# Optimization experiments

Hardware: AMD Instinct MI355X
Metric: run time of the kernel (lower is better)

## Reference

```python
import jax, jax.numpy as jnp
import numpy as np

IN_DIM, HID, OUT, B, MAX_LEN = 164, 512, 1, 1024, 128


def _uni(key, shape, fan_in):
    b = 1.0 / np.sqrt(fan_in)
    return jax.random.uniform(key, shape, jnp.float32, -b, b)


def setup_inputs() -> dict:
    rng = np.random.default_rng(0)
    sizes = rng.integers(1, MAX_LEN, size=B)  # lengths in [1, 127]
    T = int(sizes.sum())  # total ragged tokens (~65k)
    key = jax.random.key(0)
    ks = jax.random.split(key, 16)
    return {
        "segment_sizes": jnp.asarray(sizes, jnp.int32),
        "features": jax.random.normal(ks[0], (T, IN_DIM), jnp.float32),
        # encoder MLP: Linear(in,hid) -> ReLU -> Linear(hid,hid) -> ReLU
        "We0": _uni(ks[1], (HID, IN_DIM), IN_DIM), "be0": _uni(ks[2], (HID,), IN_DIM),
        "We1": _uni(ks[3], (HID, HID), HID),       "be1": _uni(ks[4], (HID,), HID),
        # single-layer LSTM, torch gate order (i, f, g, o)
        "Wih": _uni(ks[5], (4 * HID, HID), HID),   "bih": _uni(ks[6], (4 * HID,), HID),
        "Whh": _uni(ks[7], (4 * HID, HID), HID),   "bhh": _uni(ks[8], (4 * HID,), HID),
        # residual MLPs l0, l1
        "Wl0": _uni(ks[9], (HID, HID), HID),  "bl0": _uni(ks[10], (HID,), HID),
        "Wl1": _uni(ks[11], (HID, HID), HID), "bl1": _uni(ks[12], (HID,), HID),
        # decoder Linear(hid, out)
        "Wd": _uni(ks[13], (OUT, HID), HID), "bd": _uni(ks[14], (OUT,), HID),
    }


def reference(segment_sizes, features, We0, be0, We1, be1,
              Wih, bih, Whh, bhh, Wl0, bl0, Wl1, bl1, Wd, bd):
    T = features.shape[0]
    # segment encoder MLP on ragged tokens
    x = jax.nn.relu(features @ We0.T + be0)
    x = jax.nn.relu(x @ We1.T + be1)  # [T, HID]
    # pad_sequence: scatter ragged tokens into [MAX_LEN, B, HID] (zero padded)
    starts = jnp.cumsum(segment_sizes) - segment_sizes
    seg = jnp.repeat(jnp.arange(B), segment_sizes, total_repeat_length=T)
    pos = jnp.arange(T) - starts[seg]
    padded = jnp.zeros((MAX_LEN, B, HID), x.dtype).at[pos, seg].set(x)

    # LSTM scan; note: original runs the LSTM over padded zeros too and takes
    # h after the full MAX_LEN steps (no packing) -- reproduce that exactly.
    def step(carry, xt):
        h, c = carry
        g = xt @ Wih.T + bih + h @ Whh.T + bhh  # [B, 4H]
        i, f, gg, o = jnp.split(g, 4, axis=-1)
        c = jax.nn.sigmoid(f) * c + jax.nn.sigmoid(i) * jnp.tanh(gg)
        h = jax.nn.sigmoid(o) * jnp.tanh(c)
        return (h, c), None

    zeros = jnp.zeros((B, HID), x.dtype)
    (h, _), _ = jax.lax.scan(step, (zeros, zeros), padded)

    out = h  # norm is Identity
    out = jax.nn.relu(out @ Wl0.T + bl0) + out
    out = jax.nn.relu(out @ Wl1.T + bl1) + out
    out = (out @ Wd.T + bd).squeeze()  # [B]
    return out
```

## Files before the change

### kernel.cpp

```cpp
#include <hip/hip_runtime.h>
#include <hip/hip_bf16.h>

typedef __attribute__((ext_vector_type(8))) short short8;
typedef __attribute__((ext_vector_type(4))) float f32x4;

#define DEV __device__ __forceinline__

DEV short f2bf(float f){ __hip_bfloat16 h = __float2bfloat16(f); return *reinterpret_cast<short*>(&h); }
DEV float bf2f(short s){ __hip_bfloat16 h; *reinterpret_cast<short*>(&h) = s; return __bfloat162float(h); }

DEV float sigm(float x){ return 1.f/(1.f + __expf(-x)); }
DEV float tanh_f(float x){
  float ax = fabsf(x);
  float e = __expf(-2.f*ax);
  float t = (1.f - e)/(1.f + e);
  return copysignf(t, x);
}

DEV short8 llc_ld16(const short* p){
  union { unsigned long long u[2]; short8 v; } r;
  r.u[0] = __hip_atomic_load((const unsigned long long*)p,
                             __ATOMIC_RELAXED, __HIP_MEMORY_SCOPE_AGENT);
  r.u[1] = __hip_atomic_load((const unsigned long long*)(p + 4),
                             __ATOMIC_RELAXED, __HIP_MEMORY_SCOPE_AGENT);
  return r.v;
}


__global__ void k_cvt(const float* __restrict__ in, short* __restrict__ out, long n){
  long i = (long)blockIdx.x*blockDim.x + threadIdx.x;
  long st = (long)gridDim.x*blockDim.x;
  for (; i < n; i += st) out[i] = f2bf(in[i]);
}

__global__ void k_cvt_pad(const float* __restrict__ in, short* __restrict__ out,
                          int rows, int ic, int oc){
  long n = (long)rows*oc;
  long st = (long)gridDim.x*blockDim.x;
  for (long i = (long)blockIdx.x*blockDim.x + threadIdx.x; i < n; i += st){
    int r = (int)(i / oc), c = (int)(i % oc);
    out[i] = (c < ic) ? f2bf(in[(long)r*ic + c]) : (short)0;
  }
}

__global__ void k_bias2(const float* __restrict__ a, const float* __restrict__ b,
                        float* __restrict__ o, int n){
  int i = blockIdx.x*blockDim.x + threadIdx.x;
  if (i < n) o[i] = a[i] + b[i];
}

__global__ void k_scan(const int* __restrict__ sizes, int* __restrict__ starts, int B){
  __shared__ int t[1024];
  int tid = threadIdx.x;
  int v = (tid < B) ? sizes[tid] : 0;
  t[tid] = v;
  __syncthreads();
  for (int off = 1; off < 1024; off <<= 1){
    int add = (tid >= off) ? t[tid-off] : 0;
    __syncthreads();
    t[tid] += add;
    __syncthreads();
  }
  if (tid < B) starts[tid] = t[tid] - v;
}

template<bool RELU, bool RESID, bool OBF, bool OF32, bool AF32>
__global__ __launch_bounds__(256) void k_gemm(
    const void* __restrict__ Araw, int lda, int Ktrue,
    const short* __restrict__ Bw, int ldb,
    const float* __restrict__ bias,
    const float* __restrict__ R,
    short* __restrict__ Cb, float* __restrict__ Cf, int ldc,
    int M, int N, int K)
{
  constexpr int BM = 64, BN = 128, BK = 64;
  __shared__ short lA[(BK/8)*BM*8];
  __shared__ short lB[(BK/8)*BN*8];
  const short* Ab = (const short*)Araw;
  const float* Af = (const float*)Araw;
  const int tid = threadIdx.x;
  const int l = tid & 63, w = tid >> 6;
  const int lr = l & 15, lk = l >> 4;
  const int bm0 = blockIdx.x*BM, bn0 = blockIdx.y*BN;

  f32x4 acc[4][2];
  #pragma unroll
  for (int a = 0; a < 4; a++)
    #pragma unroll
    for (int b = 0; b < 2; b++) acc[a][b] = (f32x4){0.f,0.f,0.f,0.f};

  for (int k0 = 0; k0 < K; k0 += BK){
    #pragma unroll
    for (int i = 0; i < 2; i++){
      int idx = tid + i*256;
      int m = idx >> 3, kc = idx & 7;
      int gm = bm0 + m; if (gm >= M) gm = M-1;
      short8 v;
      if (AF32){
        int kb = k0 + kc*8;
        if (kb + 8 <= Ktrue){
          const float* p = Af + (long)gm*lda + kb;
          float4 f0 = *(const float4*)p;
          float4 f1 = *(const float4*)(p + 4);
          v[0]=f2bf(f0.x); v[1]=f2bf(f0.y); v[2]=f2bf(f0.z); v[3]=f2bf(f0.w);
          v[4]=f2bf(f1.x); v[5]=f2bf(f1.y); v[6]=f2bf(f1.z); v[7]=f2bf(f1.w);
        } else {
          #pragma unroll
          for (int e = 0; e < 8; e++){
            int k = kb + e;
            v[e] = (k < Ktrue) ? f2bf(Af[(long)gm*lda + k]) : (short)0;
          }
        }
      } else {
        v = *(const short8*)(Ab + (long)gm*lda + k0 + kc*8);
      }
      *(short8*)&lA[(kc*BM + m)*8] = v;
    }
    #pragma unroll
    for (int i = 0; i < 4; i++){
      int idx = tid + i*256;
      int n = idx >> 3, kc = idx & 7;
      *(short8*)&lB[(kc*BN + n)*8] = *(const short8*)(Bw + (long)(bn0+n)*ldb + k0 + kc*8);
    }
    __syncthreads();
    #pragma unroll
    for (int kb = 0; kb < 2; kb++){
      short8 af[4], bfv[2];
      #pragma unroll
      for (int mf = 0; mf < 4; mf++)
        af[mf] = *(short8*)&lA[((kb*4+lk)*BM + mf*16 + lr)*8];
      #pragma unroll
      for (int nf = 0; nf < 2; nf++)
        bfv[nf] = *(short8*)&lB[((kb*4+lk)*BN + w*32 + nf*16 + lr)*8];
      #pragma unroll
      for (int mf = 0; mf < 4; mf++)
        #pragma unroll
        for (int nf = 0; nf < 2; nf++)
          acc[mf][nf] = __builtin_amdgcn_mfma_f32_16x16x32_bf16(af[mf], bfv[nf], acc[mf][nf], 0, 0, 0);
    }
    __syncthreads();
  }

  #pragma unroll
  for (int mf = 0; mf < 4; mf++){
    #pragma unroll
    for (int nf = 0; nf < 2; nf++){
      #pragma unroll
      for (int r = 0; r < 4; r++){
        int row = bm0 + mf*16 + lk*4 + r;
        int col = bn0 + w*32 + nf*16 + lr;
        if (row < M){
          float v = acc[mf][nf][r];
          if (bias) v += bias[col];
          if (RELU) v = fmaxf(v, 0.f);
          if (RESID) v += R[(long)row*ldc + col];
          if (OBF) Cb[(long)row*ldc + col] = f2bf(v);
          if (OF32) Cf[(long)row*ldc + col] = v;
        }
      }
    }
  }
}

__global__ __launch_bounds__(256, 1) void k_lstm(
    const short* __restrict__ Whh,
    const short* __restrict__ Wih,
    const short* __restrict__ Xt,
    short* __restrict__ h0, short* __restrict__ h1,
    float* __restrict__ hF,
    const int* __restrict__ sizes, const int* __restrict__ starts,
    const float* __restrict__ bias2, unsigned int* __restrict__ cnt)
{
  __shared__ short wx[4*2*16*64*8];
  const int bid = blockIdx.x;
  const int xcd = bid & 7;
  const int q   = bid >> 3;
  const int ht  = q & 15;
  const int bm  = ((q >> 4) << 3) | xcd;
  const int tid = threadIdx.x;
  const int l = tid & 63, wid = tid >> 6;
  const int wr = wid >> 1, wc = wid & 1;
  const int lr = l & 15, lk = l >> 4;
  const int rowbase = bm*64 + wr*32;
  const int j = ht*32 + wc*16 + lr;

  for (int c = tid; c < 8192; c += 256){
    int lane = c & 63;
    int kk  = (c >> 6) & 15;
    int wcs = (c >> 10) & 1;
    int g   = c >> 11;
    int row = g*512 + ht*32 + wcs*16 + (lane & 15);
    int col = kk*32 + (lane >> 4)*8;
    *(short8*)&wx[(size_t)c*8] = *(const short8*)(Wih + (long)row*512 + col);
  }

  short8 Breg[4][16];
  #pragma unroll
  for (int g = 0; g < 4; ++g){
    const short* wp = Whh + (long)(g*512 + j)*512 + lk*8;
    #pragma unroll
    for (int kk = 0; kk < 16; ++kk)
      Breg[g][kk] = *(const short8*)(wp + kk*32);
  }

  float bz[4];
  #pragma unroll
  for (int g = 0; g < 4; ++g) bz[g] = bias2[g*512 + j];

  const int len0 = sizes[rowbase + lr];
  const int len1 = sizes[rowbase + 16 + lr];
  const long xb0 = (long)starts[rowbase + lr]*512;
  const long xb1 = (long)starts[rowbase + 16 + lr]*512;

  __syncthreads();

  float cst[2][4] = {{0.f,0.f,0.f,0.f},{0.f,0.f,0.f,0.f}};
  const int cidx = bm*128;
  const short8 z8 = {0,0,0,0,0,0,0,0};
  const int wxw = wc*16*64*8;

  #pragma unroll 1
  for (int t = 0; t < 128; ++t){
    const short* hc = (t & 1) ? h1 : h0;
    short*       hn = (t & 1) ? h0 : h1;
    const bool on0 = t < len0, on1 = t < len1;
    const short* px0 = Xt + xb0 + (on0 ? (long)t*512 : 0) + lk*8;
    const short* px1 = Xt + xb1 + (on1 ? (long)t*512 : 0) + lk*8;

    f32x4 acc[2][4];
    #pragma unroll
    for (int mf = 0; mf < 2; ++mf)
      #pragma unroll
      for (int g = 0; g < 4; ++g) acc[mf][g] = (f32x4){0.f,0.f,0.f,0.f};

    #pragma unroll
    for (int kk = 0; kk < 16; ++kk){
      short8 x0 = on0 ? *(const short8*)(px0 + kk*32) : z8;
      short8 x1 = on1 ? *(const short8*)(px1 + kk*32) : z8;
      #pragma unroll
      for (int g = 0; g < 4; ++g){
        short8 bx = *(short8*)&wx[g*(2*16*64*8) + wxw + (kk*64 + l)*8];
        acc[0][g] = __builtin_amdgcn_mfma_f32_16x16x32_bf16(x0, bx, acc[0][g], 0, 0, 0);
        acc[1][g] = __builtin_amdgcn_mfma_f32_16x16x32_bf16(x1, bx, acc[1][g], 0, 0, 0);
      }
    }

    if (t > 0){
      if (tid == 0){
        while (__hip_atomic_load(&cnt[cidx + t - 1], __ATOMIC_RELAXED,
                                 __HIP_MEMORY_SCOPE_AGENT) < 16u)
          __builtin_amdgcn_s_sleep(1);
      }
      __syncthreads();
      asm volatile("" ::: "memory");
      __builtin_amdgcn_sched_barrier(0);

      const short* ph = hc + (long)(rowbase + lr)*512 + lk*8;
      #pragma unroll
      for (int kk = 0; kk < 16; ++kk){
        short8 a0 = llc_ld16(ph + kk*32);
        short8 a1 = llc_ld16(ph + 16*512 + kk*32);
        #pragma unroll
        for (int g = 0; g < 4; ++g){
          acc[0][g] = __builtin_amdgcn_mfma_f32_16x16x32_bf16(a0, Breg[g][kk], acc[0][g], 0, 0, 0);
          acc[1][g] = __builtin_amdgcn_mfma_f32_16x16x32_bf16(a1, Breg[g][kk], acc[1][g], 0, 0, 0);
        }
      }
    }

    #pragma unroll
    for (int mf = 0; mf < 2; ++mf)
      #pragma unroll
      for (int r = 0; r < 4; ++r){
        int rb = rowbase + mf*16 + lk*4 + r;
        float ip = acc[mf][0][r] + bz[0];
        float fp = acc[mf][1][r] + bz[1];
        float gp = acc[mf][2][r] + bz[2];
        float op = acc[mf][3][r] + bz[3];
        float cn = sigm(fp)*cst[mf][r] + sigm(ip)*tanh_f(gp);
        float hv = sigm(op)*tanh_f(cn);
        cst[mf][r] = cn;
        unsigned int x16 = (unsigned short)f2bf(hv);
        unsigned int par = (unsigned int)__shfl_xor((int)x16, 1, 64);
        if (!(lr & 1)){
          unsigned int wv = x16 | (par << 16);
          __hip_atomic_store((unsigned int*)(hn + (long)rb*512 + (j & ~1)), wv,
                             __ATOMIC_RELAXED, __HIP_MEMORY_SCOPE_AGENT);
        }
        if (t == 127) hF[(long)rb*512 + j] = hv;
      }

    asm volatile("s_waitcnt vmcnt(0) lgkmcnt(0)" ::: "memory");
    __syncthreads();
    if (tid == 0)
      __hip_atomic_fetch_add(&cnt[cidx + t], 1u, __ATOMIC_RELAXED,
                             __HIP_MEMORY_SCOPE_AGENT);
  }
}

__global__ __launch_bounds__(256) void k_dec(const float* __restrict__ X,
                                             const float* __restrict__ Wd,
                                             const float* __restrict__ bd,
                                             float* __restrict__ out, int B){
  int w = threadIdx.x >> 6, l = threadIdx.x & 63;
  int row = blockIdx.x*4 + w;
  if (row >= B) return;
  float s = 0.f;
  #pragma unroll
  for (int e = 0; e < 8; e++){
    int j = l + 64*e;
    s += X[(long)row*512 + j]*Wd[j];
  }
  #pragma unroll
  for (int off = 32; off > 0; off >>= 1) s += __shfl_down(s, off);
  if (l == 0) out[row] = s + bd[0];
}


extern "C" void kernel_launch(void* const* d_in, const int* in_sizes, int n_in,
                              void* d_out, int out_size, void* d_ws, size_t ws_size,
                              hipStream_t stream)
{
  const int*   sizes = (const int*)  d_in[0];
  const float* feat  = (const float*)d_in[1];
  const float* We0   = (const float*)d_in[2];
  const float* be0   = (const float*)d_in[3];
  const float* We1   = (const float*)d_in[4];
  const float* be1   = (const float*)d_in[5];
  const float* Wih   = (const float*)d_in[6];
  const float* bih   = (const float*)d_in[7];
  const float* Whh   = (const float*)d_in[8];
  const float* bhh   = (const float*)d_in[9];
  const float* Wl0   = (const float*)d_in[10];
  const float* bl0   = (const float*)d_in[11];
  const float* Wl1   = (const float*)d_in[12];
  const float* bl1   = (const float*)d_in[13];
  const float* Wd    = (const float*)d_in[14];
  const float* bd    = (const float*)d_in[15];

  const int B = in_sizes[0];
  const int T = in_sizes[1] / 164;
  const int HID = 512;

  char* base = (char*)d_ws;
  size_t off = 0;
  auto alloc = [&](size_t bytes)->char*{
    char* p = base + off;
    off = (off + bytes + 255) & ~(size_t)255;
    return p;
  };

  int*          starts = (int*)         alloc((size_t)B*4);
  float*        bias2  = (float*)       alloc(2048*4);
  unsigned int* cnt    = (unsigned int*)alloc(16*128*4);
  short* We0b   = (short*)alloc((size_t)512*192*2);
  short* We1b   = (short*)alloc((size_t)512*512*2);
  short* Wihb   = (short*)alloc((size_t)2048*512*2);
  short* Whhb   = (short*)alloc((size_t)2048*512*2);
  short* Wl0b   = (short*)alloc((size_t)512*512*2);
  short* Wl1b   = (short*)alloc((size_t)512*512*2);
  short* hA     = (short*)alloc((size_t)B*HID*2);
  short* hB     = (short*)alloc((size_t)B*HID*2);
  float* hF     = (float*)alloc((size_t)B*HID*4);
  float* r1     = (float*)alloc((size_t)B*HID*4);
  short* r1b    = (short*)alloc((size_t)B*HID*2);
  float* r2     = (float*)alloc((size_t)B*HID*4);
  short* X0b    = (short*)alloc((size_t)T*512*2);
  short* Xb     = (short*)alloc((size_t)T*512*2);
  (void)ws_size; (void)n_in; (void)out_size;

  hipMemsetAsync(cnt, 0, (size_t)16*128*4, stream);

  k_scan<<<1, 1024, 0, stream>>>(sizes, starts, B);
  k_bias2<<<8, 256, 0, stream>>>(bih, bhh, bias2, 2048);

  auto grd = [](long n){ long g = (n + 255)/256; return (int)(g > 4096 ? 4096 : g); };
  k_cvt_pad<<<grd(512l*192), 256, 0, stream>>>(We0, We0b, 512, 164, 192);
  k_cvt<<<grd(512l*512), 256, 0, stream>>>(We1, We1b, 512l*512);
  k_cvt<<<grd(2048l*512), 256, 0, stream>>>(Wih, Wihb, 2048l*512);
  k_cvt<<<grd(2048l*512), 256, 0, stream>>>(Whh, Whhb, 2048l*512);
  k_cvt<<<grd(512l*512), 256, 0, stream>>>(Wl0, Wl0b, 512l*512);
  k_cvt<<<grd(512l*512), 256, 0, stream>>>(Wl1, Wl1b, 512l*512);

  int mt = (T + 63)/64;
  k_gemm<true,false,true,false,true><<<dim3(mt, 4), 256, 0, stream>>>(
      (const void*)feat, 164, 164, We0b, 192, be0, nullptr, X0b, nullptr, 512, T, 512, 192);
  k_gemm<true,false,true,false,false><<<dim3(mt, 4), 256, 0, stream>>>(
      (const void*)X0b, 512, 512, We1b, 512, be1, nullptr, Xb, nullptr, 512, T, 512, 512);

  k_lstm<<<256, 256, 0, stream>>>(Whhb, Wihb, Xb, hA, hB, hF,
                                  sizes, starts, bias2, cnt);

  k_gemm<true,true,true,true,true><<<dim3(16, 4), 256, 0, stream>>>(
      (const void*)hF, 512, 512, Wl0b, 512, bl0, hF, r1b, r1, 512, B, 512, 512);
  k_gemm<true,true,false,true,false><<<dim3(16, 4), 256, 0, stream>>>(
      (const void*)r1b, 512, 512, Wl1b, 512, bl1, r1, nullptr, r2, 512, B, 512, 512);

  k_dec<<<B/4, 256, 0, stream>>>(r2, Wd, bd, (float*)d_out, B);
}
```

Measured before the change: 2.293 ms.

## Replace per-step atomic counter with per-block step flags and batch h loads

The cross-block LSTM step barrier changes from a shared atomic counter incremented by each of 16 blocks to per-block flag words that each block overwrites with its step number. A whole wavefront polls the 16 flags in parallel, which avoids contention from atomic read-modify-write. The h loads are also hoisted ahead of the MFMA loop so all global loads issue before any compute, and the final step skips the h store and barrier. Holding all h loads in flight raises register pressure in a kernel already keeping Whh in registers.

```diff
diff --git a/kernel.cpp b/kernel.cpp
--- a/kernel.cpp
+++ b/kernel.cpp
@@ -169,7 +169,7 @@
     short* __restrict__ h0, short* __restrict__ h1,
     float* __restrict__ hF,
     const int* __restrict__ sizes, const int* __restrict__ starts,
-    const float* __restrict__ bias2, unsigned int* __restrict__ cnt)
+    const float* __restrict__ bias2, unsigned int* __restrict__ flags)
 {
   __shared__ short wx[4*2*16*64*8];
   const int bid = blockIdx.x;
@@ -183,6 +183,7 @@
   const int lr = l & 15, lk = l >> 4;
   const int rowbase = bm*64 + wr*32;
   const int j = ht*32 + wc*16 + lr;
+  const int fb = bm*16;
 
   for (int c = tid; c < 8192; c += 256){
     int lane = c & 63;
@@ -215,7 +216,6 @@
   __syncthreads();
 
   float cst[2][4] = {{0.f,0.f,0.f,0.f},{0.f,0.f,0.f,0.f}};
-  const int cidx = bm*128;
   const short8 z8 = {0,0,0,0,0,0,0,0};
   const int wxw = wc*16*64*8;
 
@@ -246,24 +246,32 @@
     }
 
     if (t > 0){
-      if (tid == 0){
-        while (__hip_atomic_load(&cnt[cidx + t - 1], __ATOMIC_RELAXED,
-                                 __HIP_MEMORY_SCOPE_AGENT) < 16u)
-          __builtin_amdgcn_s_sleep(1);
+      if (wid == 0){
+        const unsigned int want = (unsigned int)t;
+        while (true){
+          unsigned int v = __hip_atomic_load(&flags[fb + (l & 15)],
+                                             __ATOMIC_RELAXED, __HIP_MEMORY_SCOPE_AGENT);
+          if (__all(v >= want)) break;
+          __builtin_amdgcn_s_sleep(2);
+        }
       }
       __syncthreads();
       asm volatile("" ::: "memory");
       __builtin_amdgcn_sched_barrier(0);
 
       const short* ph = hc + (long)(rowbase + lr)*512 + lk*8;
+      short8 ha0[16], ha1[16];
       #pragma unroll
       for (int kk = 0; kk < 16; ++kk){
-        short8 a0 = llc_ld16(ph + kk*32);
-        short8 a1 = llc_ld16(ph + 16*512 + kk*32);
+        ha0[kk] = llc_ld16(ph + kk*32);
+        ha1[kk] = llc_ld16(ph + 16*512 + kk*32);
+      }
+      #pragma unroll
+      for (int kk = 0; kk < 16; ++kk){
         #pragma unroll
         for (int g = 0; g < 4; ++g){
-          acc[0][g] = __builtin_amdgcn_mfma_f32_16x16x32_bf16(a0, Breg[g][kk], acc[0][g], 0, 0, 0);
-          acc[1][g] = __builtin_amdgcn_mfma_f32_16x16x32_bf16(a1, Breg[g][kk], acc[1][g], 0, 0, 0);
+          acc[0][g] = __builtin_amdgcn_mfma_f32_16x16x32_bf16(ha0[kk], Breg[g][kk], acc[0][g], 0, 0, 0);
+          acc[1][g] = __builtin_amdgcn_mfma_f32_16x16x32_bf16(ha1[kk], Breg[g][kk], acc[1][g], 0, 0, 0);
         }
       }
     }
@@ -280,21 +288,26 @@
         float cn = sigm(fp)*cst[mf][r] + sigm(ip)*tanh_f(gp);
         float hv = sigm(op)*tanh_f(cn);
         cst[mf][r] = cn;
-        unsigned int x16 = (unsigned short)f2bf(hv);
-        unsigned int par = (unsigned int)__shfl_xor((int)x16, 1, 64);
-        if (!(lr & 1)){
-          unsigned int wv = x16 | (par << 16);
-          __hip_atomic_store((unsigned int*)(hn + (long)rb*512 + (j & ~1)), wv,
-                             __ATOMIC_RELAXED, __HIP_MEMORY_SCOPE_AGENT);
+        if (t < 127){
+          unsigned int x16 = (unsigned short)f2bf(hv);
+          unsigned int par = (unsigned int)__shfl_xor((int)x16, 1, 64);
+          if (!(lr & 1)){
+            unsigned int wv = x16 | (par << 16);
+            __hip_atomic_store((unsigned int*)(hn + (long)rb*512 + (j & ~1)), wv,
+                               __ATOMIC_RELAXED, __HIP_MEMORY_SCOPE_AGENT);
+          }
+        } else {
+          hF[(long)rb*512 + j] = hv;
         }
-        if (t == 127) hF[(long)rb*512 + j] = hv;
-      }
-
-    asm volatile("s_waitcnt vmcnt(0) lgkmcnt(0)" ::: "memory");
-    __syncthreads();
-    if (tid == 0)
-      __hip_atomic_fetch_add(&cnt[cidx + t], 1u, __ATOMIC_RELAXED,
-                             __HIP_MEMORY_SCOPE_AGENT);
+      }
+
+    if (t < 127){
+      asm volatile("s_waitcnt vmcnt(0) lgkmcnt(0)" ::: "memory");
+      __syncthreads();
+      if (tid == 0)
+        __hip_atomic_store(&flags[fb + ht], (unsigned int)(t + 1),
+                           __ATOMIC_RELAXED, __HIP_MEMORY_SCOPE_AGENT);
+    }
   }
 }
 
@@ -352,7 +365,7 @@
 
   int*          starts = (int*)         alloc((size_t)B*4);
   float*        bias2  = (float*)       alloc(2048*4);
-  unsigned int* cnt    = (unsigned int*)alloc(16*128*4);
+  unsigned int* flags  = (unsigned int*)alloc(256*4);
   short* We0b   = (short*)alloc((size_t)512*192*2);
   short* We1b   = (short*)alloc((size_t)512*512*2);
   short* Wihb   = (short*)alloc((size_t)2048*512*2);
@@ -369,7 +382,7 @@
   short* Xb     = (short*)alloc((size_t)T*512*2);
   (void)ws_size; (void)n_in; (void)out_size;
 
-  hipMemsetAsync(cnt, 0, (size_t)16*128*4, stream);
+  hipMemsetAsync(flags, 0, 256*4, stream);
 
   k_scan<<<1, 1024, 0, stream>>>(sizes, starts, B);
   k_bias2<<<8, 256, 0, stream>>>(bih, bhh, bias2, 2048);
@@ -389,7 +402,7 @@
       (const void*)X0b, 512, 512, We1b, 512, be1, nullptr, Xb, nullptr, 512, T, 512, 512);
 
   k_lstm<<<256, 256, 0, stream>>>(Whhb, Wihb, Xb, hA, hB, hF,
-                                  sizes, starts, bias2, cnt);
+                                  sizes, starts, bias2, flags);
 
   k_gemm<true,true,true,true,true><<<dim3(16, 4), 256, 0, stream>>>(
       (const void*)hF, 512, 512, Wl0b, 512, bl0, hF, r1b, r1, 512, B, 512, 512);
```

Measured after the change: 2.301 ms. Within noise of the previous version (+0.3%).
